# Performance work log

Hardware: AMD Instinct MI355X
Metric: run time of the kernel (lower is better)

Reference implementation:

```python
import jax, jax.numpy as jnp
import numpy as np

N, D = 8192, 256
SIM_THRESHOLD = 0.85
EPS = 1e-12  # matches torch F.normalize eps


def setup_inputs() -> dict:
    key = jax.random.key(0)
    k1, k2, k3 = jax.random.split(key, 3)
    return {
        "cls_embeddings": jax.random.normal(k1, (N, D), dtype=jnp.float32),
        "w1": jax.random.normal(k2, (4, 16), dtype=jnp.float32) * 0.5,
        "b1": jnp.zeros((16,), dtype=jnp.float32),
        "w2": jax.random.normal(k3, (16, 1), dtype=jnp.float32) * 0.25,
        "b2": jnp.zeros((1,), dtype=jnp.float32),
    }


def _similarity_features(cls_embeddings):
    # 4-dim features from the pairwise cosine-similarity matrix.
    n = cls_embeddings.shape[0]
    norm = jnp.maximum(jnp.linalg.norm(cls_embeddings, axis=-1, keepdims=True), EPS)
    normed = cls_embeddings / norm
    sim = normed @ normed.T                      # [n, n]
    eye = jnp.eye(n, dtype=bool)
    off = ~eye
    n_pairs = n * (n - 1)
    max_sim = jnp.where(off, sim, -jnp.inf).max()
    mean_sim = jnp.where(off, sim, 0.0).sum() / n_pairs
    frac_above = (jnp.where(off, sim, 0.0) > SIM_THRESHOLD).sum() / n_pairs

    # Connected components over edges {sim > 0.85} == union-find cluster count.
    # Min-label propagation + pointer jumping (Shiloach-Vishkin style),
    # converges in O(log n) iterations.
    adj = (jax.lax.stop_gradient(sim) > SIM_THRESHOLD) | eye  # include self
    labels0 = jnp.arange(n, dtype=jnp.int32)

    def body(_, labels):
        nb_min = jnp.where(adj, labels[None, :], n).min(axis=1).astype(jnp.int32)
        labels = jnp.minimum(labels, nb_min)
        return labels[labels]  # pointer jump

    iters = int(np.ceil(np.log2(max(n, 2)))) + 3
    labels = jax.lax.fori_loop(0, iters, body, labels0)
    cluster_count = (labels == labels0).sum() / n  # roots are component minima

    return jnp.stack([max_sim, mean_sim,
                      frac_above.astype(jnp.float32),
                      cluster_count.astype(jnp.float32)])


def reference(cls_embeddings, w1, b1, w2, b2):
    feats = _similarity_features(cls_embeddings)[None, :]          # [1, 4]
    h = jax.nn.gelu(feats @ w1 + b1, approximate=False)            # [1, 16]
    score = jax.nn.sigmoid(h @ w2 + b2)                            # [1, 1]
    return score
```

## Files before the change

kernel.cpp:

```cpp
#include <hip/hip_runtime.h>
#include <math.h>

#define NROWS 8192
#define DIM   256
#define K2    256
#define NTB   64
#define NTRI  2080
#define SIM_THR 0.85f

#define A2_OFF   1024
#define EDGE_OFF (1024 + NROWS * K2 * 2)

typedef _Float16 half8 __attribute__((ext_vector_type(8)));
typedef float f32x4 __attribute__((ext_vector_type(4)));

__device__ inline void load_lds16(const void* g, void* l) {
    __builtin_amdgcn_global_load_lds((const __attribute__((address_space(1))) void*)g,
                                     (__attribute__((address_space(3))) void*)l, 16, 0, 0);
}

__device__ inline void atomicMaxF(float* addr, float val) {
    if (val >= 0.f) atomicMax((int*)addr, __float_as_int(val));
    else            atomicMin((unsigned int*)addr, __float_as_uint(val));
}

__global__ __launch_bounds__(256) void prep_kernel(const float* __restrict__ x,
                                                   unsigned short* __restrict__ a2,
                                                   float* wsf) {
    if (blockIdx.x == 0 && threadIdx.x == 0) {
        wsf[0] = -INFINITY; wsf[1] = 0.f;
        ((unsigned int*)wsf)[2] = 0u; ((unsigned int*)wsf)[3] = 0u;
    }
    int row  = blockIdx.x * 4 + (threadIdx.x >> 6);
    int lane = threadIdx.x & 63;
    float4 v = ((const float4*)(x + (size_t)row * DIM))[lane];
    float ss = v.x * v.x + v.y * v.y + v.z * v.z + v.w * v.w;
    #pragma unroll
    for (int off = 32; off; off >>= 1) ss += __shfl_xor(ss, off);
    float norm = fmaxf(sqrtf(ss), 1e-12f);
    float f[4] = {v.x / norm, v.y / norm, v.z / norm, v.w / norm};
    unsigned short h[4];
    #pragma unroll
    for (int j = 0; j < 4; ++j)
        h[j] = __builtin_bit_cast(unsigned short, (_Float16)f[j]);
    *(ushort4*)(a2 + (size_t)row * K2 + lane * 4) = make_ushort4(h[0], h[1], h[2], h[3]);
}

__global__ __launch_bounds__(256) void sim_kernel(const unsigned short* __restrict__ a2,
                                                  float* wsf, int2* edges, int cap) {
    int bid = blockIdx.x;
    int idx = (bid & 7) * (NTRI / 8) + (bid >> 3);
    int bi = (int)((sqrtf(8.f * idx + 1.f) - 1.f) * 0.5f);
    while ((bi + 1) * (bi + 2) / 2 <= idx) ++bi;
    while (bi * (bi + 1) / 2 > idx) --bi;
    int bj = idx - bi * (bi + 1) / 2;
    int i0 = bi * 128, j0 = bj * 128;

    __shared__ __align__(16) char As[4][128 * 128];
    __shared__ __align__(16) char Bs[4][128 * 128];
    __shared__ float sred[12];

    int t = threadIdx.x, lane = t & 63, w = t >> 6;
    int wr = w >> 1, wc = w & 1;

    f32x4 acc[4][4] = {};

    int perm = ((lane & 7) ^ (lane >> 3)) * 16;
    const char* gA = (const char*)a2 + (size_t)(i0 + w * 32 + (lane >> 3)) * 512 + perm;
    const char* gB = (const char*)a2 + (size_t)(j0 + w * 32 + (lane >> 3)) * 512 + perm;
    int ldsW = w * 32 * 128;

    #pragma unroll
    for (int kc = 0; kc < 4; ++kc) {
        #pragma unroll
        for (int q = 0; q < 4; ++q) {
            load_lds16(gA + kc * 128 + q * 4096, As[kc] + ldsW + q * 1024);
            load_lds16(gB + kc * 128 + q * 4096, Bs[kc] + ldsW + q * 1024);
        }
    }
    asm volatile("s_waitcnt vmcnt(0)" ::: "memory");
    __builtin_amdgcn_s_barrier();

    int rbA = (wr * 64 + (lane & 15)) * 128;
    int rbB = (wc * 64 + (lane & 15)) * 128;
    int kx  = (lane & 7) << 4;
    int kb0 = (lane >> 4) << 4;

    #pragma unroll
    for (int kc = 0; kc < 4; ++kc) {
        const char* A = As[kc];
        const char* B = Bs[kc];
        #pragma unroll
        for (int ks = 0; ks < 2; ++ks) {
            int kb = (ks * 64 + kb0) ^ kx;
            half8 af[4], bf[4];
            #pragma unroll
            for (int m = 0; m < 4; ++m) {
                af[m] = *(const half8*)(A + rbA + m * 2048 + kb);
                bf[m] = *(const half8*)(B + rbB + m * 2048 + kb);
            }
            #pragma unroll
            for (int m = 0; m < 4; ++m)
                #pragma unroll
                for (int n = 0; n < 4; ++n)
                    acc[m][n] = __builtin_amdgcn_mfma_f32_16x16x32_f16(af[m], bf[n], acc[m][n], 0, 0, 0);
        }
    }

    bool diagT = (bi == bj);
    float        wgt  = diagT ? 1.f : 2.f;
    unsigned int wgtu = diagT ? 1u : 2u;
    float lmax = -INFINITY, lsum = 0.f;
    unsigned int lcnt = 0;
    #pragma unroll
    for (int m = 0; m < 4; ++m) {
        #pragma unroll
        for (int n = 0; n < 4; ++n) {
            #pragma unroll
            for (int j = 0; j < 4; ++j) {
                float s = acc[m][n][j];
                int gi = i0 + wr * 64 + m * 16 + (lane >> 4) * 4 + j;
                int gj = j0 + wc * 64 + n * 16 + (lane & 15);
                if (gi != gj) {
                    lmax = fmaxf(lmax, s);
                    lsum += s;
                    if (s > SIM_THR) {
                        lcnt++;
                        unsigned int e = atomicAdd(&((unsigned int*)wsf)[3], 1u);
                        if (e < (unsigned int)cap) edges[e] = make_int2(gi, gj);
                    }
                }
            }
        }
    }
    #pragma unroll
    for (int off = 32; off; off >>= 1) {
        lmax = fmaxf(lmax, __shfl_xor(lmax, off));
        lsum += __shfl_xor(lsum, off);
        lcnt += __shfl_xor(lcnt, off);
    }
    if (lane == 0) { sred[w] = lmax; sred[4 + w] = lsum; ((unsigned int*)sred)[8 + w] = lcnt; }
    __syncthreads();
    if (t == 0) {
        float bm = fmaxf(fmaxf(sred[0], sred[1]), fmaxf(sred[2], sred[3]));
        float bs = sred[4] + sred[5] + sred[6] + sred[7];
        unsigned int bc = ((unsigned int*)sred)[8] + ((unsigned int*)sred)[9]
                        + ((unsigned int*)sred)[10] + ((unsigned int*)sred)[11];
        atomicMaxF(&wsf[0], bm);
        atomicAdd(&wsf[1], bs * wgt);
        if (bc) atomicAdd(&((unsigned int*)wsf)[2], bc * wgtu);
    }
}

__global__ __launch_bounds__(1024) void finalize_kernel(const float* wsf, const int2* edges, int cap,
                                                        const float* __restrict__ w1,
                                                        const float* __restrict__ b1,
                                                        const float* __restrict__ w2,
                                                        const float* __restrict__ b2,
                                                        float* __restrict__ out) {
    __shared__ int lab[NROWS];
    __shared__ int tmp[NROWS];
    __shared__ int wsum[16];
    int t = threadIdx.x;
    for (int i = t; i < NROWS; i += 1024) lab[i] = i;
    unsigned int ec = ((const unsigned int*)wsf)[3];
    if (ec > (unsigned int)cap) ec = (unsigned int)cap;
    __syncthreads();

    if (ec > 0) {
        for (int it = 0; it < 16; ++it) {
            for (int i = t; i < NROWS; i += 1024) tmp[i] = lab[i];
            __syncthreads();
            for (unsigned int e = t; e < ec; e += 1024) {
                int u = edges[e].x, v = edges[e].y;
                atomicMin(&tmp[u], lab[v]);
                atomicMin(&tmp[v], lab[u]);
            }
            __syncthreads();
            for (int i = t; i < NROWS; i += 1024) lab[i] = tmp[tmp[i]];
            __syncthreads();
        }
    }

    int lc = 0;
    for (int i = t; i < NROWS; i += 1024) lc += (lab[i] == i);
    #pragma unroll
    for (int off = 32; off; off >>= 1) lc += __shfl_xor(lc, off);
    if ((t & 63) == 0) wsum[t >> 6] = lc;
    __syncthreads();

    if (t == 0) {
        int roots = 0;
        #pragma unroll
        for (int q = 0; q < 16; ++q) roots += wsum[q];
        const float n_pairs = 67100672.0f;
        float feats[4];
        feats[0] = wsf[0];
        feats[1] = wsf[1] / n_pairs;
        feats[2] = (float)((const unsigned int*)wsf)[2] / n_pairs;
        feats[3] = (float)roots / (float)NROWS;
        float acc2 = b2[0];
        for (int j = 0; j < 16; ++j) {
            float hj = b1[j];
            #pragma unroll
            for (int i = 0; i < 4; ++i) hj = fmaf(feats[i], w1[i * 16 + j], hj);
            float g = 0.5f * hj * (1.0f + erff(hj * 0.70710678118f));
            acc2 = fmaf(g, w2[j], acc2);
        }
        out[0] = 1.0f / (1.0f + expf(-acc2));
    }
}

extern "C" void kernel_launch(void* const* d_in, const int* in_sizes, int n_in,
                              void* d_out, int out_size, void* d_ws, size_t ws_size,
                              hipStream_t stream) {
    const float* cls = (const float*)d_in[0];
    const float* w1  = (const float*)d_in[1];
    const float* b1  = (const float*)d_in[2];
    const float* w2  = (const float*)d_in[3];
    const float* b2  = (const float*)d_in[4];
    float* out = (float*)d_out;

    float* wsf = (float*)d_ws;
    unsigned short* a2 = (unsigned short*)((char*)d_ws + A2_OFF);
    int2* edges = (int2*)((char*)d_ws + EDGE_OFF);
    long long avail = (long long)ws_size - (long long)EDGE_OFF;
    int cap = (int)(avail > 0 ? (avail / 8 > 4194304 ? 4194304 : avail / 8) : 0);

    prep_kernel<<<NROWS / 4, 256, 0, stream>>>(cls, a2, wsf);
    sim_kernel<<<NTRI, 256, 0, stream>>>(a2, wsf, edges, cap);
    finalize_kernel<<<1, 1024, 0, stream>>>(wsf, edges, cap, w1, b1, w2, b2, out);
}
```

Measured before the change: 134.8 us.

## Load MFMA operands directly from global memory, dropping LDS staging

The sim kernel no longer stages the 128x256 A and B tiles in 128 KB of shared memory. Each wave now reads its fp16 fragments straight from global memory (L2/cache) into registers, and launch bounds now request 3 blocks per CU. This removes the LDS fill, the barrier and the shared-memory footprint that limited occupancy. In exchange, each wave re-fetches data that was shared across waves, which adds global/L2 traffic and exposes load latency with no explicit prefetch.

```diff
diff --git a/kernel.cpp b/kernel.cpp
--- a/kernel.cpp
+++ b/kernel.cpp
@@ -14,11 +14,6 @@
 typedef _Float16 half8 __attribute__((ext_vector_type(8)));
 typedef float f32x4 __attribute__((ext_vector_type(4)));
 
-__device__ inline void load_lds16(const void* g, void* l) {
-    __builtin_amdgcn_global_load_lds((const __attribute__((address_space(1))) void*)g,
-                                     (__attribute__((address_space(3))) void*)l, 16, 0, 0);
-}
-
 __device__ inline void atomicMaxF(float* addr, float val) {
     if (val >= 0.f) atomicMax((int*)addr, __float_as_int(val));
     else            atomicMin((unsigned int*)addr, __float_as_uint(val));
@@ -46,8 +41,8 @@
     *(ushort4*)(a2 + (size_t)row * K2 + lane * 4) = make_ushort4(h[0], h[1], h[2], h[3]);
 }
 
-__global__ __launch_bounds__(256) void sim_kernel(const unsigned short* __restrict__ a2,
-                                                  float* wsf, int2* edges, int cap) {
+__global__ __launch_bounds__(256, 3) void sim_kernel(const unsigned short* __restrict__ a2,
+                                                     float* wsf, int2* edges, int cap) {
     int bid = blockIdx.x;
     int idx = (bid & 7) * (NTRI / 8) + (bid >> 3);
     int bi = (int)((sqrtf(8.f * idx + 1.f) - 1.f) * 0.5f);
@@ -56,8 +51,6 @@
     int bj = idx - bi * (bi + 1) / 2;
     int i0 = bi * 128, j0 = bj * 128;
 
-    __shared__ __align__(16) char As[4][128 * 128];
-    __shared__ __align__(16) char Bs[4][128 * 128];
     __shared__ float sred[12];
 
     int t = threadIdx.x, lane = t & 63, w = t >> 6;
@@ -65,46 +58,26 @@
 
     f32x4 acc[4][4] = {};
 
-    int perm = ((lane & 7) ^ (lane >> 3)) * 16;
-    const char* gA = (const char*)a2 + (size_t)(i0 + w * 32 + (lane >> 3)) * 512 + perm;
-    const char* gB = (const char*)a2 + (size_t)(j0 + w * 32 + (lane >> 3)) * 512 + perm;
-    int ldsW = w * 32 * 128;
-
-    #pragma unroll
-    for (int kc = 0; kc < 4; ++kc) {
-        #pragma unroll
-        for (int q = 0; q < 4; ++q) {
-            load_lds16(gA + kc * 128 + q * 4096, As[kc] + ldsW + q * 1024);
-            load_lds16(gB + kc * 128 + q * 4096, Bs[kc] + ldsW + q * 1024);
-        }
-    }
-    asm volatile("s_waitcnt vmcnt(0)" ::: "memory");
-    __builtin_amdgcn_s_barrier();
-
-    int rbA = (wr * 64 + (lane & 15)) * 128;
-    int rbB = (wc * 64 + (lane & 15)) * 128;
-    int kx  = (lane & 7) << 4;
-    int kb0 = (lane >> 4) << 4;
-
-    #pragma unroll
-    for (int kc = 0; kc < 4; ++kc) {
-        const char* A = As[kc];
-        const char* B = Bs[kc];
-        #pragma unroll
-        for (int ks = 0; ks < 2; ++ks) {
-            int kb = (ks * 64 + kb0) ^ kx;
-            half8 af[4], bf[4];
+    const char* base = (const char*)a2;
+    int rowA = i0 + wr * 64 + (lane & 15);
+    int rowB = j0 + wc * 64 + (lane & 15);
+    int koff = (lane >> 4) * 16;
+    const char* pA = base + (size_t)rowA * 512 + koff;
+    const char* pB = base + (size_t)rowB * 512 + koff;
+
+    #pragma unroll
+    for (int ks = 0; ks < 8; ++ks) {
+        half8 af[4], bf[4];
+        #pragma unroll
+        for (int m = 0; m < 4; ++m) {
+            af[m] = *(const half8*)(pA + m * (16 * 512) + ks * 64);
+            bf[m] = *(const half8*)(pB + m * (16 * 512) + ks * 64);
+        }
+        #pragma unroll
+        for (int m = 0; m < 4; ++m)
             #pragma unroll
-            for (int m = 0; m < 4; ++m) {
-                af[m] = *(const half8*)(A + rbA + m * 2048 + kb);
-                bf[m] = *(const half8*)(B + rbB + m * 2048 + kb);
-            }
-            #pragma unroll
-            for (int m = 0; m < 4; ++m)
-                #pragma unroll
-                for (int n = 0; n < 4; ++n)
-                    acc[m][n] = __builtin_amdgcn_mfma_f32_16x16x32_f16(af[m], bf[n], acc[m][n], 0, 0, 0);
-        }
+            for (int n = 0; n < 4; ++n)
+                acc[m][n] = __builtin_amdgcn_mfma_f32_16x16x32_f16(af[m], bf[n], acc[m][n], 0, 0, 0);
     }
 
     bool diagT = (bi == bj);
```

New measurement: 155.6 us. 15.5% more time.
